# Kernel optimization log

Measured on AMD Instinct MI355X. Metric: run time of the kernel, lower is better.

Reference implementation:

```python
import jax, jax.numpy as jnp
import numpy as np

B, T = 128, 100
NOISE_STD = 0.1  # deterministic=False path

def leaky(x, slope):
    return jnp.where(x >= 0, x, slope * x)

def setup_inputs() -> dict:
    key = jax.random.key(0)
    ks = jax.random.split(key, 24)
    s = 0.02
    d = {}
    d["input_data"] = jax.random.normal(ks[0], (B, T, 3, 3), jnp.float32)
    d["eps"] = jax.random.normal(ks[1], (B, 64), jnp.float32)
    d["noise_eps"] = jax.random.normal(ks[2], (T, B, 4), jnp.float32)
    d["proj_W"] = jax.random.normal(ks[3], (4096, 9), jnp.float32) * s
    d["proj_b"] = jnp.zeros((4096,), jnp.float32)
    d["lstm_Wih"] = jax.random.normal(ks[4], (512, 4096), jnp.float32) * s
    d["lstm_Whh"] = jax.random.normal(ks[5], (512, 128), jnp.float32) * s
    d["lstm_bih"] = jnp.zeros((512,), jnp.float32)
    d["lstm_bhh"] = jnp.zeros((512,), jnp.float32)
    d["mu_W"] = jax.random.normal(ks[6], (64, 128), jnp.float32) * s
    d["mu_b"] = jnp.zeros((64,), jnp.float32)
    d["lv_W"] = jax.random.normal(ks[7], (64, 128), jnp.float32) * s
    d["lv_b"] = jnp.zeros((64,), jnp.float32)
    d["fcin_W"] = jax.random.normal(ks[8], (256, 64), jnp.float32) * s
    d["fcin_b"] = jnp.zeros((256,), jnp.float32)
    d["gru_Wih"] = jax.random.normal(ks[9], (783, 261), jnp.float32) * s
    d["gru_Whh"] = jax.random.normal(ks[10], (783, 261), jnp.float32) * s
    d["gru_bih"] = jnp.zeros((783,), jnp.float32)
    d["gru_bhh"] = jnp.zeros((783,), jnp.float32)
    d["jf_W1"] = jax.random.normal(ks[11], (64, 261), jnp.float32) * s
    d["jf_b1"] = jnp.zeros((64,), jnp.float32)
    d["jf_W2"] = jax.random.normal(ks[12], (9, 64), jnp.float32) * s
    d["jf_b2"] = jnp.zeros((9,), jnp.float32)
    return d

def reference(input_data, eps, noise_eps, proj_W, proj_b, lstm_Wih, lstm_Whh,
              lstm_bih, lstm_bhh, mu_W, mu_b, lv_W, lv_b, fcin_W, fcin_b,
              gru_Wih, gru_Whh, gru_bih, gru_bhh, jf_W1, jf_b1, jf_W2, jf_b2):
    b, t = input_data.shape[0], input_data.shape[1]
    pose = input_data.reshape(b, t, 9)
    # pose_projection: Linear(9, 4096) + LeakyReLU(0.1)
    proj = leaky(jnp.einsum('btj,kj->btk', pose, proj_W) + proj_b, 0.1)  # (B,T,4096)

    # LSTM over time, take final hidden state. PyTorch gate order: i,f,g,o.
    # Precompute input projections for all steps.
    x_gates = jnp.einsum('btk,gk->tbg', proj, lstm_Wih) + lstm_bih + lstm_bhh  # (T,B,512)
    hdim = 128
    def lstm_step(carry, xg):
        h, c = carry
        g = xg + h @ lstm_Whh.T  # (B,512)
        i, f, gg, o = jnp.split(g, 4, axis=-1)
        i, f, o = jax.nn.sigmoid(i), jax.nn.sigmoid(f), jax.nn.sigmoid(o)
        c = f * c + i * jnp.tanh(gg)
        h = o * jnp.tanh(c)
        return (h, c), None
    h0 = jnp.zeros((b, hdim), proj.dtype)
    (h_T, _), _ = jax.lax.scan(lstm_step, (h0, h0), x_gates)

    # VAE head (dropout in eval mode = identity)
    mu = leaky(h_T @ mu_W.T + mu_b, 0.1)
    logvar = jnp.clip(leaky(h_T @ lv_W.T + lv_b, 0.1), -10.0, 10.0)
    std = jnp.exp(0.5 * logvar)
    embedding = mu + eps * std

    x = embedding @ fcin_W.T + fcin_b  # (B,256)

    # Decoder GRU loop. PyTorch gate order: r,z,n; h' = (1-z)*n + z*h.
    noise = noise_eps * NOISE_STD  # (T,B,4)
    time_steps = (jnp.arange(t, dtype=x.dtype) / (t - 1))[:, None, None] * jnp.ones((t, b, 1), x.dtype)
    inp_seq = jnp.concatenate([jnp.broadcast_to(x[None], (t, b, 256)), noise, time_steps], axis=-1)  # (T,B,261)
    gx_seq = jnp.einsum('tbk,gk->tbg', inp_seq, gru_Wih) + gru_bih  # (T,B,783)

    def gru_step(h, gx):
        gh = h @ gru_Whh.T + gru_bhh
        gx_r, gx_z, gx_n = jnp.split(gx, 3, axis=-1)
        gh_r, gh_z, gh_n = jnp.split(gh, 3, axis=-1)
        r = jax.nn.sigmoid(gx_r + gh_r)
        z = jax.nn.sigmoid(gx_z + gh_z)
        n = jnp.tanh(gx_n + r * gh_n)
        h = (1.0 - z) * n + z * h
        frame = jax.nn.sigmoid(leaky(h @ jf_W1.T + jf_b1, 0.2) @ jf_W2.T + jf_b2)
        return h, frame

    h0g = jnp.zeros((b, 261), x.dtype)
    _, frames = jax.lax.scan(gru_step, h0g, gx_seq)  # (T,B,9)
    outputs = frames.transpose(1, 0, 2).reshape(b, t, 3, 3)
    return outputs, mu, logvar
```

## Files before the change

### kernel.cpp

```cpp
#include <hip/hip_runtime.h>
#include <hip/hip_bf16.h>

typedef float f32x4 __attribute__((ext_vector_type(4)));
typedef short s16x8 __attribute__((ext_vector_type(8)));

__device__ __forceinline__ float pv_sigm(float x){ return 1.0f/(1.0f + __expf(-x)); }
__device__ __forceinline__ float pv_tanh(float x){ float e = __expf(2.0f*x); return 1.0f - 2.0f/(e + 1.0f); }

__device__ __forceinline__ unsigned short pv_f2b(float x){
  union { float f; unsigned u; } c; c.f = x;
  unsigned r = (c.u + 0x7fffu + ((c.u >> 16) & 1u)) >> 16;
  return (unsigned short)r;
}
__device__ __forceinline__ unsigned pv_pack2(float a, float b){
  return ((unsigned)pv_f2b(b) << 16) | (unsigned)pv_f2b(a);
}
__device__ __forceinline__ float pv_lo(unsigned u){
  union { unsigned u; float f; } c; c.u = u << 16; return c.f;
}
__device__ __forceinline__ float pv_hi(unsigned u){
  union { unsigned u; float f; } c; c.u = u & 0xffff0000u; return c.f;
}

__device__ __forceinline__ unsigned char pv_fp8(float x){
  union { float f; unsigned u; } c; c.f = x;
  unsigned s = (c.u >> 24) & 0x80u;
  unsigned au = c.u & 0x7fffffffu;
  if (au == 0u) return (unsigned char)s;
  int ex = (int)(au >> 23) - 127;
  if (ex < -6) ex = -6;
  union { unsigned u; float f; } iv; iv.u = (unsigned)(3 - ex + 127) << 23;
  union { unsigned u; float f; } a;  a.u = au;
  int q = (int)rintf(a.f * iv.f);
  if (q >= 16) { q >>= 1; ex += 1; }
  unsigned bits;
  if (ex == -6 && q < 8) bits = (unsigned)q;
  else bits = (unsigned)(((ex + 7) << 3) | (q - 8));
  return (unsigned char)(s | bits);
}

#if defined(__has_builtin)
#if __has_builtin(__builtin_amdgcn_cvt_pk_fp8_f32)
#define PV_HW_FP8 1
#endif
#endif
__device__ __forceinline__ unsigned char pv_fp8_fast(float x){
#ifdef PV_HW_FP8
  return (unsigned char)__builtin_amdgcn_cvt_pk_fp8_f32(x, x, 0, false);
#else
  return pv_fp8(x);
#endif
}

__global__ void pv_prep_gru8(const float* Whh, const float* Wih,
                             unsigned long long* wfp8){
  int idx = blockIdx.x*256 + threadIdx.x;
  if (idx >= 29376) return;
  int T = idx / 576;
  int rem = idx - T*576;
  int c = rem >> 6;
  int l = rem & 63;
  int l16 = l & 15;
  int quad = l >> 4;
  int jb = T / 3;
  int ty = T - jb*3;
  int j = jb*16 + l16;
  int g = ty*261 + j;
  unsigned long long v = 0ull;
  #pragma unroll
  for (int e = 0; e < 8; ++e) {
    int k = c*32 + quad*8 + e;
    float w = 0.0f;
    if (j < 261) {
      if (k < 261) w = Whh[g*261 + k];
      else if (k < 266 && ty < 2) w = Wih[g*261 + 256 + (k - 261)];
    }
    v |= (unsigned long long)pv_fp8(8.0f*w) << (8*e);
  }
  wfp8[idx] = v;
}

__global__ __launch_bounds__(256) void pv_prep_wih(
    const float* __restrict__ Wih, unsigned* __restrict__ wihb)
{
  const int idx = blockIdx.x*256 + threadIdx.x;
  if (idx >= 262144) return;
  const float* src = Wih + idx*8;
  float4 a = *(const float4*)(src);
  float4 b = *(const float4*)(src + 4);
  uint4 o;
  o.x = pv_pack2(a.x, a.y);
  o.y = pv_pack2(a.z, a.w);
  o.z = pv_pack2(b.x, b.y);
  o.w = pv_pack2(b.z, b.w);
  *(uint4*)(wihb + idx*4) = o;
}

__global__ __launch_bounds__(512, 1) void pv_gemm4(
    const float* __restrict__ pose, const float* __restrict__ projW,
    const float* __restrict__ projb, const unsigned* __restrict__ wihb,
    const float* __restrict__ bih, const float* __restrict__ bhh,
    float* __restrict__ xg)
{
  __shared__ __align__(16) unsigned As2[128*20];
  __shared__ __align__(16) unsigned Bs2[2][256*20];
  __shared__ __align__(16) float Ws2[2][320];

  const int tid = threadIdx.x;
  const int m0 = blockIdx.x * 128;
  const int n0 = blockIdx.y * 256;
  const int wave = tid >> 6, lane = tid & 63;
  const int wm = wave >> 2, wn = wave & 3;
  const int l16 = lane & 15, quad = lane >> 4;
  const int rl = tid >> 2, kq = tid & 3;
  const int rb = tid >> 1, hb = tid & 1;

  float p[9];
  {
    const float* pr = pose + (m0 + rl)*9;
    #pragma unroll
    for (int j = 0; j < 9; ++j) p[j] = pr[j];
  }

  if (tid < 320) {
    Ws2[0][tid < 288 ? ((tid >> 5)*32 + (tid & 31)) : tid] =
        (tid < 288) ? projW[(tid & 31)*9 + (tid >> 5)] : projb[tid - 288];
  }
  {
    const unsigned* src = wihb + (n0 + rb)*2048 + hb*8;
    *(uint4*)(&Bs2[0][rb*20 + hb*8])     = *(const uint4*)(src);
    *(uint4*)(&Bs2[0][rb*20 + hb*8 + 4]) = *(const uint4*)(src + 4);
  }
  __syncthreads();

  f32x4 acc[4][4];
  #pragma unroll
  for (int i = 0; i < 4; ++i)
    #pragma unroll
    for (int j = 0; j < 4; ++j) acc[i][j] = (f32x4){0.f,0.f,0.f,0.f};

  for (int kk = 0; kk < 128; ++kk) {
    const int cur = kk & 1, nxt = cur ^ 1;
    const int kn = kk + 1;

    uint4 bn0, bn1; float wv = 0.0f;
    if (kn < 128) {
      const unsigned* bsrc = wihb + (n0 + rb)*2048 + kn*16 + hb*8;
      bn0 = *(const uint4*)(bsrc);
      bn1 = *(const uint4*)(bsrc + 4);
      if (tid < 320)
        wv = (tid < 288) ? projW[kn*288 + (tid & 31)*9 + (tid >> 5)]
                         : projb[kn*32 + (tid - 288)];
    }

    {
      const float* W = Ws2[cur];
      f32x4 slo = *(const f32x4*)(W + 288 + kq*8);
      f32x4 shi = *(const f32x4*)(W + 292 + kq*8);
      #pragma unroll
      for (int j = 0; j < 9; ++j) {
        f32x4 wlo = *(const f32x4*)(W + j*32 + kq*8);
        f32x4 whi = *(const f32x4*)(W + j*32 + kq*8 + 4);
        slo += p[j]*wlo;
        shi += p[j]*whi;
      }
      #pragma unroll
      for (int e = 0; e < 4; ++e) {
        slo[e] = fmaxf(slo[e], 0.1f*slo[e]);
        shi[e] = fmaxf(shi[e], 0.1f*shi[e]);
      }
      uint4 av;
      av.x = pv_pack2(slo[0], slo[1]);
      av.y = pv_pack2(slo[2], slo[3]);
      av.z = pv_pack2(shi[0], shi[1]);
      av.w = pv_pack2(shi[2], shi[3]);
      *(uint4*)(&As2[rl*20 + kq*4]) = av;
    }
    __syncthreads();

    {
      const unsigned short* As16 = (const unsigned short*)As2;
      const unsigned short* Bs16 = (const unsigned short*)Bs2[cur];
      s16x8 af[4];
      #pragma unroll
      for (int i = 0; i < 4; ++i)
        af[i] = *(const s16x8*)(As16 + (wm*64 + i*16 + l16)*40 + quad*8);
      #pragma unroll
      for (int j = 0; j < 4; ++j) {
        s16x8 bv = *(const s16x8*)(Bs16 + (wn*64 + j*16 + l16)*40 + quad*8);
        #pragma unroll
        for (int i = 0; i < 4; ++i)
          acc[i][j] = __builtin_amdgcn_mfma_f32_16x16x32_bf16(af[i], bv, acc[i][j], 0, 0, 0);
      }
    }

    if (kn < 128) {
      *(uint4*)(&Bs2[nxt][rb*20 + hb*8])     = bn0;
      *(uint4*)(&Bs2[nxt][rb*20 + hb*8 + 4]) = bn1;
      if (tid < 320)
        Ws2[nxt][tid < 288 ? ((tid >> 5)*32 + (tid & 31)) : tid] = wv;
    }
    __syncthreads();
  }

  #pragma unroll
  for (int j = 0; j < 4; ++j) {
    int col = n0 + wn*64 + j*16 + l16;
    float bsum = bih[col] + bhh[col];
    #pragma unroll
    for (int i = 0; i < 4; ++i) {
      #pragma unroll
      for (int r = 0; r < 4; ++r) {
        int row = m0 + wm*64 + i*16 + quad*4 + r;
        int bb = row / 100;
        int tt = row - bb*100;
        xg[(tt*128 + bb)*512 + col] = acc[i][j][r] + bsum;
      }
    }
  }
}

__global__ __launch_bounds__(256) void pv_gemm(
    const float* pose, const float* projW, const float* projb,
    const float* Wih, const float* bih, const float* bhh,
    float* xg)
{
  __shared__ __align__(16) unsigned As[128*24];
  __shared__ __align__(16) unsigned Bs[128*24];
  __shared__ float Ws[320];

  const int tid = threadIdx.x;
  const int m0 = blockIdx.x * 128;
  const int n0 = blockIdx.y * 128;

  const int rl = tid >> 1;
  const int kh = tid & 1;
  float p0,p1,p2,p3,p4,p5,p6,p7,p8;
  {
    const float* pr = pose + (m0 + rl) * 9;
    p0=pr[0]; p1=pr[1]; p2=pr[2]; p3=pr[3]; p4=pr[4];
    p5=pr[5]; p6=pr[6]; p7=pr[7]; p8=pr[8];
  }

  const int wave = tid >> 6;
  const int lane = tid & 63;
  const int wm = wave >> 1, wn = wave & 1;
  const int l16 = lane & 15, quad = lane >> 4;

  f32x4 acc[4][4];
  #pragma unroll
  for (int i = 0; i < 4; ++i)
    #pragma unroll
    for (int j = 0; j < 4; ++j) acc[i][j] = (f32x4){0.f,0.f,0.f,0.f};

  for (int kk = 0; kk < 128; ++kk) {
    __syncthreads();
    for (int idx = tid; idx < 320; idx += 256)
      Ws[idx] = (idx < 288) ? projW[kk*288 + idx] : projb[kk*32 + (idx - 288)];
    #pragma unroll
    for (int i = 0; i < 8; ++i) {
      int q = tid + i*256;
      int nl = q >> 4;
      int kp = q & 15;
      const float* src = Wih + (n0 + nl)*4096 + kk*32 + kp*2;
      Bs[nl*24 + kp] = pv_pack2(src[0], src[1]);
    }
    __syncthreads();
    {
      const int kbase = kh*16;
      const float* wbase = Ws + kbase*9;
      float av[16];
      #pragma unroll
      for (int u = 0; u < 16; ++u) {
        const float* wr = wbase + u*9;
        float s = Ws[288 + kbase + u]
                + p0*wr[0] + p1*wr[1] + p2*wr[2] + p3*wr[3] + p4*wr[4]
                + p5*wr[5] + p6*wr[6] + p7*wr[7] + p8*wr[8];
        av[u] = fmaxf(s, 0.1f*s);
      }
      #pragma unroll
      for (int q = 0; q < 8; ++q)
        As[rl*24 + kh*8 + q] = pv_pack2(av[2*q], av[2*q+1]);
    }
    __syncthreads();
    const unsigned short* As16 = (const unsigned short*)As;
    const unsigned short* Bs16 = (const unsigned short*)Bs;
    s16x8 af[4], bfv[4];
    #pragma unroll
    for (int i = 0; i < 4; ++i)
      af[i] = *(const s16x8*)(As16 + (wm*64 + i*16 + l16)*48 + quad*8);
    #pragma unroll
    for (int j = 0; j < 4; ++j)
      bfv[j] = *(const s16x8*)(Bs16 + (wn*64 + j*16 + l16)*48 + quad*8);
    #pragma unroll
    for (int i = 0; i < 4; ++i)
      #pragma unroll
      for (int j = 0; j < 4; ++j)
        acc[i][j] = __builtin_amdgcn_mfma_f32_16x16x32_bf16(af[i], bfv[j], acc[i][j], 0, 0, 0);
  }
  #pragma unroll
  for (int j = 0; j < 4; ++j) {
    int col = n0 + wn*64 + j*16 + l16;
    float bsum = bih[col] + bhh[col];
    #pragma unroll
    for (int i = 0; i < 4; ++i) {
      #pragma unroll
      for (int r = 0; r < 4; ++r) {
        int row = m0 + wm*64 + i*16 + quad*4 + r;
        int bb = row / 100;
        int tt = row - bb*100;
        xg[(tt*128 + bb)*512 + col] = acc[i][j][r] + bsum;
      }
    }
  }
}

__global__ __launch_bounds__(512, 1) void pv_lstm2(
    const float* __restrict__ xg, const float* __restrict__ Whh,
    float* __restrict__ hT)
{
  __shared__ __align__(16) unsigned short Hs2[2][16*136];
  const int tid = threadIdx.x;
  const int wv = tid >> 6;
  const int lane = tid & 63;
  const int l16 = lane & 15, quad = lane >> 4;
  const int m0 = blockIdx.x * 16;
  const int j = wv*16 + l16;

  s16x8 bfr[4][4];
  #pragma unroll
  for (int ty = 0; ty < 4; ++ty) {
    const int g = ty*128 + j;
    #pragma unroll
    for (int c = 0; c < 4; ++c) {
      s16x8 v;
      #pragma unroll
      for (int e = 0; e < 8; ++e)
        v[e] = (short)pv_f2b(Whh[g*128 + c*32 + quad*8 + e]);
      bfr[ty][c] = v;
    }
  }
  for (int i = tid; i < 2*16*136; i += 512) ((unsigned short*)Hs2)[i] = 0;

  float cst[4] = {0.f, 0.f, 0.f, 0.f};
  const float* xbase = xg + (m0 + quad*4)*512 + j;

  float xv[4][4];
  #pragma unroll
  for (int r = 0; r < 4; ++r)
    #pragma unroll
    for (int ty = 0; ty < 4; ++ty)
      xv[r][ty] = xbase[(0*128 + r)*512 + ty*128];
  __syncthreads();

  for (int t = 0; t < 100; ++t) {
    const int cur = t & 1, nxt = cur ^ 1;
    float xn[4][4];
    if (t < 99) {
      #pragma unroll
      for (int r = 0; r < 4; ++r)
        #pragma unroll
        for (int ty = 0; ty < 4; ++ty)
          xn[r][ty] = xbase[((t+1)*128 + r)*512 + ty*128];
    }
    f32x4 acc[4];
    #pragma unroll
    for (int ty = 0; ty < 4; ++ty) acc[ty] = (f32x4){0.f,0.f,0.f,0.f};
    #pragma unroll
    for (int c = 0; c < 4; ++c) {
      s16x8 a = *(const s16x8*)(&Hs2[cur][l16*136 + c*32 + quad*8]);
      #pragma unroll
      for (int ty = 0; ty < 4; ++ty)
        acc[ty] = __builtin_amdgcn_mfma_f32_16x16x32_bf16(a, bfr[ty][c], acc[ty], 0, 0, 0);
    }
    #pragma unroll
    for (int r = 0; r < 4; ++r) {
      float gi = acc[0][r] + xv[r][0];
      float gf = acc[1][r] + xv[r][1];
      float gg = acc[2][r] + xv[r][2];
      float go = acc[3][r] + xv[r][3];
      float c_ = pv_sigm(gf)*cst[r] + pv_sigm(gi)*pv_tanh(gg);
      cst[r] = c_;
      float h = pv_sigm(go)*pv_tanh(c_);
      Hs2[nxt][(quad*4 + r)*136 + j] = pv_f2b(h);
      if (t == 99) hT[(m0 + quad*4 + r)*128 + j] = h;
    }
    if (t < 99) {
      #pragma unroll
      for (int r = 0; r < 4; ++r)
        #pragma unroll
        for (int ty = 0; ty < 4; ++ty)
          xv[r][ty] = xn[r][ty];
    }
    __syncthreads();
  }
}

__global__ __launch_bounds__(64) void pv_head(
    const float* hT, const float* eps,
    const float* muW, const float* mub,
    const float* lvW, const float* lvb,
    const float* fcW, const float* fcb,
    float* xvec, float* out)
{
  __shared__ float hrow[128];
  __shared__ float emb[64];
  const int b = blockIdx.x, j = threadIdx.x;
  hrow[j] = hT[b*128 + j];
  hrow[j + 64] = hT[b*128 + 64 + j];
  __syncthreads();
  float sm = mub[j], sl = lvb[j];
  for (int k = 0; k < 128; ++k) {
    sm += hrow[k]*muW[j*128 + k];
    sl += hrow[k]*lvW[j*128 + k];
  }
  float mu = fmaxf(sm, 0.1f*sm);
  float lv = fmaxf(sl, 0.1f*sl);
  lv = fminf(fmaxf(lv, -10.0f), 10.0f);
  float em = mu + eps[b*64 + j]*__expf(0.5f*lv);
  emb[j] = em;
  out[115200 + b*64 + j] = mu;
  out[123392 + b*64 + j] = lv;
  __syncthreads();
  for (int c4 = 0; c4 < 4; ++c4) {
    int c = c4*64 + j;
    float s = fcb[c];
    for (int k = 0; k < 64; ++k) s += emb[k]*fcW[c*64 + k];
    xvec[b*256 + c] = s;
  }
}

__global__ __launch_bounds__(256) void pv_gxbase(
    const float* xvec, const float* Wih,
    const float* bih, const float* bhh, float* gxb)
{
  __shared__ float xs[8*256];
  const int tid = threadIdx.x;
  const int bg = blockIdx.x;
  const int gg = blockIdx.y;
  for (int i = tid; i < 2048; i += 256) xs[i] = xvec[bg*2048 + i];
  __syncthreads();
  const int g = gg*256 + tid;
  if (g >= 783) return;
  float bias = bih[g] + ((g < 522) ? bhh[g] : 0.0f);
  float a0=bias,a1=bias,a2=bias,a3=bias,a4=bias,a5=bias,a6=bias,a7=bias;
  const float* wr = Wih + g*261;
  for (int k = 0; k < 256; ++k) {
    float w = wr[k];
    a0 += xs[0*256 + k]*w; a1 += xs[1*256 + k]*w;
    a2 += xs[2*256 + k]*w; a3 += xs[3*256 + k]*w;
    a4 += xs[4*256 + k]*w; a5 += xs[5*256 + k]*w;
    a6 += xs[6*256 + k]*w; a7 += xs[7*256 + k]*w;
  }
  gxb[(bg*8 + 0)*783 + g] = a0; gxb[(bg*8 + 1)*783 + g] = a1;
  gxb[(bg*8 + 2)*783 + g] = a2; gxb[(bg*8 + 3)*783 + g] = a3;
  gxb[(bg*8 + 4)*783 + g] = a4; gxb[(bg*8 + 5)*783 + g] = a5;
  gxb[(bg*8 + 6)*783 + g] = a6; gxb[(bg*8 + 7)*783 + g] = a7;
}

__global__ __launch_bounds__(512, 1) void pv_gru5(
    const float* __restrict__ gxb, const unsigned long long* __restrict__ wfp8,
    const float* __restrict__ Wih, const float* __restrict__ bhh,
    const float* __restrict__ noise, float* __restrict__ hseq)
{
  __shared__ __align__(16) unsigned long long Bl[27*9*64];
  __shared__ __align__(16) unsigned char A2[16*296];
  __shared__ __align__(16) float Ds[4*792];
  const int tid = threadIdx.x;
  const int wv = tid >> 6;
  const int lane = tid & 63;
  const int l16 = lane & 15, quad = lane >> 4;
  const int m0 = blockIdx.x * 4;
  const int tailOwner = (wv >= 5);

  long bfr[3][9];
  #pragma unroll
  for (int s = 0; s < 3; ++s)
    #pragma unroll
    for (int c = 0; c < 9; ++c)
      bfr[s][c] = (long)wfp8[((3*wv + s)*9 + c)*64 + lane];
  #pragma unroll
  for (int s = 0; s < 3; ++s)
    #pragma unroll
    for (int c = 0; c < 9; ++c)
      asm volatile("" : "+v"(bfr[s][c]));

  const int r_u = tid & 3;
  const int j1 = tid >> 2;
  const int j2 = 128 + j1;
  const int hasE3 = (tid < 20);
  const int j3 = 256 + (tid >> 2);
  float gx1[3], gx2[3], gx3[3], wn1[5], wn2[5], wn3[5];
  float bh1, bh2, bh3 = 0.f, h1 = 0.f, h2 = 0.f, h3 = 0.f;
  {
    const float* gb = gxb + (m0 + r_u)*783;
    gx1[0] = gb[j1]; gx1[1] = gb[261 + j1]; gx1[2] = gb[522 + j1];
    gx2[0] = gb[j2]; gx2[1] = gb[261 + j2]; gx2[2] = gb[522 + j2];
    const float* w1 = Wih + (522 + j1)*261 + 256;
    wn1[0] = 0.1f*w1[0]; wn1[1] = 0.1f*w1[1]; wn1[2] = 0.1f*w1[2];
    wn1[3] = 0.1f*w1[3]; wn1[4] = w1[4];
    const float* w2 = Wih + (522 + j2)*261 + 256;
    wn2[0] = 0.1f*w2[0]; wn2[1] = 0.1f*w2[1]; wn2[2] = 0.1f*w2[2];
    wn2[3] = 0.1f*w2[3]; wn2[4] = w2[4];
    bh1 = bhh[522 + j1];
    bh2 = bhh[522 + j2];
    #pragma unroll
    for (int k = 0; k < 3; ++k) gx3[k] = 0.f;
    #pragma unroll
    for (int k = 0; k < 5; ++k) wn3[k] = 0.f;
    if (hasE3) {
      gx3[0] = gb[j3]; gx3[1] = gb[261 + j3]; gx3[2] = gb[522 + j3];
      const float* w3 = Wih + (522 + j3)*261 + 256;
      wn3[0] = 0.1f*w3[0]; wn3[1] = 0.1f*w3[1]; wn3[2] = 0.1f*w3[2];
      wn3[3] = 0.1f*w3[3]; wn3[4] = w3[4];
      bh3 = bhh[522 + j3];
    }
  }

  for (int i = tid; i < 27*9*64; i += 512) Bl[i] = wfp8[24*9*64 + i];
  for (int i = tid; i < 4736; i += 512) A2[i] = 0;
  __syncthreads();
  if (tid < 20) {
    const int m = tid/5, i = tid - (tid/5)*5;
    float v = (i < 4) ? noise[(m0 + m)*4 + i]*0.1f : 0.0f;
    A2[m*296 + 261 + i] = pv_fp8(4.0f*v);
  }
  __syncthreads();

  const float inv32 = 1.0f/32.0f;
  const float* nptr = noise + (m0 + r_u)*4;
  for (int t = 0; t < 100; ++t) {
    const float4 ne = *(const float4*)(nptr + t*512);

    f32x4 acc[7];
    #pragma unroll
    for (int s = 0; s < 7; ++s) acc[s] = (f32x4){0,0,0,0};
    #pragma unroll
    for (int c = 0; c < 9; ++c) {
      const long a = *(const long*)(&A2[l16*296 + c*32 + quad*8]);
      acc[0] = __builtin_amdgcn_mfma_f32_16x16x32_fp8_fp8(a, bfr[0][c], acc[0], 0, 0, 0);
      acc[1] = __builtin_amdgcn_mfma_f32_16x16x32_fp8_fp8(a, bfr[1][c], acc[1], 0, 0, 0);
      acc[2] = __builtin_amdgcn_mfma_f32_16x16x32_fp8_fp8(a, bfr[2][c], acc[2], 0, 0, 0);
      const long b3 = (long)Bl[((3*wv + 0)*9 + c)*64 + lane];
      const long b4 = (long)Bl[((3*wv + 1)*9 + c)*64 + lane];
      const long b5 = (long)Bl[((3*wv + 2)*9 + c)*64 + lane];
      acc[3] = __builtin_amdgcn_mfma_f32_16x16x32_fp8_fp8(a, b3, acc[3], 0, 0, 0);
      acc[4] = __builtin_amdgcn_mfma_f32_16x16x32_fp8_fp8(a, b4, acc[4], 0, 0, 0);
      acc[5] = __builtin_amdgcn_mfma_f32_16x16x32_fp8_fp8(a, b5, acc[5], 0, 0, 0);
      if (tailOwner) {
        const long b6 = (long)Bl[((24 + (wv - 5))*9 + c)*64 + lane];
        acc[6] = __builtin_amdgcn_mfma_f32_16x16x32_fp8_fp8(a, b6, acc[6], 0, 0, 0);
      }
    }
    if (quad == 0) {
      #pragma unroll
      for (int s = 0; s < 3; ++s) {
        const int g = s*261 + wv*16 + l16;
        #pragma unroll
        for (int r = 0; r < 4; ++r) Ds[r*792 + g] = acc[s][r];
      }
      #pragma unroll
      for (int s = 0; s < 3; ++s) {
        const int g = s*261 + (8 + wv)*16 + l16;
        #pragma unroll
        for (int r = 0; r < 4; ++r) Ds[r*792 + g] = acc[3 + s][r];
      }
      if (tailOwner && l16 < 5) {
        const int g = (wv - 5)*261 + 256 + l16;
        #pragma unroll
        for (int r = 0; r < 4; ++r) Ds[r*792 + g] = acc[6][r];
      }
    }
    __syncthreads();

    {
      const float tv = (float)t * (1.0f/99.0f);
      const float* dsr = Ds + r_u*792;
      {
        float Dr = dsr[j1]*inv32 + gx1[0];
        float Dz = dsr[261 + j1]*inv32 + gx1[1];
        float Dn = dsr[522 + j1]*inv32;
        float nterm = ne.x*wn1[0] + ne.y*wn1[1] + ne.z*wn1[2]
                    + ne.w*wn1[3] + tv*wn1[4];
        float r_ = pv_sigm(Dr);
        float z_ = pv_sigm(Dz);
        float n_ = pv_tanh(gx1[2] + nterm + r_*(Dn + bh1));
        h1 = (1.0f - z_)*n_ + z_*h1;
        hseq[(t*128 + m0 + r_u)*261 + j1] = h1;
        A2[r_u*296 + j1] = pv_fp8_fast(4.0f*h1);
      }
      {
        float Dr = dsr[j2]*inv32 + gx2[0];
        float Dz = dsr[261 + j2]*inv32 + gx2[1];
        float Dn = dsr[522 + j2]*inv32;
        float nterm = ne.x*wn2[0] + ne.y*wn2[1] + ne.z*wn2[2]
                    + ne.w*wn2[3] + tv*wn2[4];
        float r_ = pv_sigm(Dr);
        float z_ = pv_sigm(Dz);
        float n_ = pv_tanh(gx2[2] + nterm + r_*(Dn + bh2));
        h2 = (1.0f - z_)*n_ + z_*h2;
        hseq[(t*128 + m0 + r_u)*261 + j2] = h2;
        A2[r_u*296 + j2] = pv_fp8_fast(4.0f*h2);
      }
      if (hasE3) {
        float Dr = dsr[j3]*inv32 + gx3[0];
        float Dz = dsr[261 + j3]*inv32 + gx3[1];
        float Dn = dsr[522 + j3]*inv32;
        float nterm = ne.x*wn3[0] + ne.y*wn3[1] + ne.z*wn3[2]
                    + ne.w*wn3[3] + tv*wn3[4];
        float r_ = pv_sigm(Dr);
        float z_ = pv_sigm(Dz);
        float n_ = pv_tanh(gx3[2] + nterm + r_*(Dn + bh3));
        h3 = (1.0f - z_)*n_ + z_*h3;
        hseq[(t*128 + m0 + r_u)*261 + j3] = h3;
        A2[r_u*296 + j3] = pv_fp8_fast(4.0f*h3);
      }
    }
    if (t < 99 && tid >= 40 && tid < 60) {
      const int k = tid - 40;
      const int m = k/5, i = k - (k/5)*5;
      float v = (i < 4) ? noise[((t+1)*128 + m0 + m)*4 + i]*0.1f
                        : (t+1)*(1.0f/99.0f);
      A2[m*296 + 261 + i] = pv_fp8(4.0f*v);
    }
    __syncthreads();
  }
}

__global__ __launch_bounds__(256) void pv_frames(
    const float* hseq, const float* W1, const float* b1,
    const float* W2, const float* b2, float* out)
{
  __shared__ __align__(16) float h16[16*264];
  __shared__ unsigned w1p[64*133];
  __shared__ float f1s[16*66];
  __shared__ float w2s[576];
  const int tid = threadIdx.x;
  const int r0 = blockIdx.x * 16;
  for (int i = tid; i < 16*264; i += 256) {
    int r = i / 264, k = i - r*264;
    h16[i] = (k < 261) ? hseq[(r0 + r)*261 + k] : 0.0f;
  }
  for (int i = tid; i < 64*131; i += 256) {
    int c = i/131, kp = i - (i/131)*131;
    int k = kp*2;
    float a0 = W1[c*261 + k];
    float a1 = (k + 1 < 261) ? W1[c*261 + k + 1] : 0.0f;
    w1p[c*133 + kp] = pv_pack2(a0, a1);
  }
  for (int i = tid; i < 576; i += 256) w2s[i] = W2[i];
  __syncthreads();
  #pragma unroll
  for (int e = 0; e < 4; ++e) {
    const int el = tid + e*256;
    const int r = el >> 6, c = el & 63;
    float s = b1[c];
    const unsigned* wp = w1p + c*133;
    const float* hr = h16 + r*264;
    for (int kp = 0; kp < 131; ++kp) {
      unsigned w = wp[kp];
      s += pv_lo(w)*hr[2*kp] + pv_hi(w)*hr[2*kp + 1];
    }
    f1s[r*66 + c] = fmaxf(s, 0.2f*s);
  }
  __syncthreads();
  if (tid < 144) {
    const int r = tid/9, oc = tid - (tid/9)*9;
    float s = b2[oc];
    const float* fr = f1s + r*66;
    const float* w = w2s + oc*64;
    #pragma unroll 8
    for (int k = 0; k < 64; ++k) s += fr[k]*w[k];
    const int rt = r0 + r;
    const int tt = rt >> 7, bb = rt & 127;
    out[bb*900 + tt*9 + oc] = pv_sigm(s);
  }
}

extern "C" __attribute__((visibility("default")))
void kernel_launch(void* const* d_in, const int* in_sizes, int n_in,
                   void* d_out, int out_size, void* d_ws, size_t ws_size,
                   hipStream_t stream)
{
  (void)in_sizes; (void)n_in; (void)out_size;
  const float* input_data = (const float*)d_in[0];
  const float* eps        = (const float*)d_in[1];
  const float* noise_eps  = (const float*)d_in[2];
  const float* proj_W     = (const float*)d_in[3];
  const float* proj_b     = (const float*)d_in[4];
  const float* lstm_Wih   = (const float*)d_in[5];
  const float* lstm_Whh   = (const float*)d_in[6];
  const float* lstm_bih   = (const float*)d_in[7];
  const float* lstm_bhh   = (const float*)d_in[8];
  const float* mu_W       = (const float*)d_in[9];
  const float* mu_b       = (const float*)d_in[10];
  const float* lv_W       = (const float*)d_in[11];
  const float* lv_b       = (const float*)d_in[12];
  const float* fcin_W     = (const float*)d_in[13];
  const float* fcin_b     = (const float*)d_in[14];
  const float* gru_Wih    = (const float*)d_in[15];
  const float* gru_Whh    = (const float*)d_in[16];
  const float* gru_bih    = (const float*)d_in[17];
  const float* gru_bhh    = (const float*)d_in[18];
  const float* jf_W1      = (const float*)d_in[19];
  const float* jf_b1      = (const float*)d_in[20];
  const float* jf_W2      = (const float*)d_in[21];
  const float* jf_b2      = (const float*)d_in[22];

  char* w = (char*)d_ws;
  float*              xg   = (float*)(w);
  unsigned long long* wfp8 = (unsigned long long*)(w + 26214400);
  float*              hT   = (float*)(w + 26449408);
  float*              xvec = (float*)(w + 26514944);
  float*              gxb  = (float*)(w + 26646016);
  float*              hseq = (float*)(w + 27046912);
  unsigned*           wihb = (unsigned*)(w + 40410112);
  float*              outf = (float*)d_out;

  const int use_split = (ws_size >= (size_t)44604416ull);

  pv_prep_gru8<<<115, 256, 0, stream>>>(gru_Whh, gru_Wih, wfp8);
  if (use_split) {
    pv_prep_wih<<<1024, 256, 0, stream>>>(lstm_Wih, wihb);
    pv_gemm4<<<dim3(100, 2), 512, 0, stream>>>(input_data, proj_W, proj_b, wihb,
                                               lstm_bih, lstm_bhh, xg);
  } else {
    pv_gemm<<<dim3(100, 4), 256, 0, stream>>>(input_data, proj_W, proj_b,
                                              lstm_Wih, lstm_bih, lstm_bhh, xg);
  }
  pv_lstm2<<<8, 512, 0, stream>>>(xg, lstm_Whh, hT);
  pv_head<<<128, 64, 0, stream>>>(hT, eps, mu_W, mu_b, lv_W, lv_b,
                                  fcin_W, fcin_b, xvec, outf);
  pv_gxbase<<<dim3(16, 4), 256, 0, stream>>>(xvec, gru_Wih, gru_bih, gru_bhh, gxb);
  pv_gru5<<<32, 512, 0, stream>>>(gxb, wfp8, gru_Wih, gru_bhh, noise_eps, hseq);
  pv_frames<<<800, 256, 0, stream>>>(hseq, jf_W1, jf_b1, jf_W2, jf_b2, outf);
}
```

Before: 747.8 us.

## Split LSTM batch across 32 blocks with 4 rows each and LDS gate exchange

The LSTM recurrence kernel now gives each block 4 batch rows instead of 16, launching 32 blocks instead of 8 to use more CUs. The MFMA still computes a 16-row tile, but only rows from quad 0 are valid; those gate pre-activations go through shared memory so that every thread does the elementwise cell update for one (row, unit) pair. This adds an extra barrier per step and a single-buffered H, in exchange for 4x less serial elementwise work per thread and more parallelism across the chip.

```diff
diff --git a/kernel.cpp b/kernel.cpp
--- a/kernel.cpp
+++ b/kernel.cpp
@@ -315,16 +315,17 @@
   }
 }
 
-__global__ __launch_bounds__(512, 1) void pv_lstm2(
+__global__ __launch_bounds__(512, 1) void pv_lstm3(
     const float* __restrict__ xg, const float* __restrict__ Whh,
     float* __restrict__ hT)
 {
-  __shared__ __align__(16) unsigned short Hs2[2][16*136];
+  __shared__ __align__(16) unsigned short Hs[16*136];
+  __shared__ __align__(16) float Ds[4*512];
   const int tid = threadIdx.x;
   const int wv = tid >> 6;
   const int lane = tid & 63;
   const int l16 = lane & 15, quad = lane >> 4;
-  const int m0 = blockIdx.x * 16;
+  const int m0 = blockIdx.x * 4;
   const int j = wv*16 + l16;
 
   s16x8 bfr[4][4];
@@ -340,57 +341,59 @@
       bfr[ty][c] = v;
     }
   }
-  for (int i = tid; i < 2*16*136; i += 512) ((unsigned short*)Hs2)[i] = 0;
-
-  float cst[4] = {0.f, 0.f, 0.f, 0.f};
-  const float* xbase = xg + (m0 + quad*4)*512 + j;
-
-  float xv[4][4];
-  #pragma unroll
-  for (int r = 0; r < 4; ++r)
-    #pragma unroll
-    for (int ty = 0; ty < 4; ++ty)
-      xv[r][ty] = xbase[(0*128 + r)*512 + ty*128];
+  for (int i = tid; i < 16*136; i += 512) Hs[i] = 0;
+
+  const int r_u = tid >> 7;
+  const int j_u = tid & 127;
+  float cst = 0.0f;
+  const float* xbase = xg + (m0 + r_u)*512 + j_u;
+
+  float xv[4];
+  #pragma unroll
+  for (int ty = 0; ty < 4; ++ty) xv[ty] = xbase[ty*128];
   __syncthreads();
 
   for (int t = 0; t < 100; ++t) {
-    const int cur = t & 1, nxt = cur ^ 1;
-    float xn[4][4];
+    float xn[4];
     if (t < 99) {
       #pragma unroll
-      for (int r = 0; r < 4; ++r)
-        #pragma unroll
-        for (int ty = 0; ty < 4; ++ty)
-          xn[r][ty] = xbase[((t+1)*128 + r)*512 + ty*128];
+      for (int ty = 0; ty < 4; ++ty)
+        xn[ty] = xbase[(t+1)*65536 + ty*128];
     }
     f32x4 acc[4];
     #pragma unroll
     for (int ty = 0; ty < 4; ++ty) acc[ty] = (f32x4){0.f,0.f,0.f,0.f};
     #pragma unroll
     for (int c = 0; c < 4; ++c) {
-      s16x8 a = *(const s16x8*)(&Hs2[cur][l16*136 + c*32 + quad*8]);
+      s16x8 a = *(const s16x8*)(&Hs[l16*136 + c*32 + quad*8]);
       #pragma unroll
       for (int ty = 0; ty < 4; ++ty)
         acc[ty] = __builtin_amdgcn_mfma_f32_16x16x32_bf16(a, bfr[ty][c], acc[ty], 0, 0, 0);
     }
-    #pragma unroll
-    for (int r = 0; r < 4; ++r) {
-      float gi = acc[0][r] + xv[r][0];
-      float gf = acc[1][r] + xv[r][1];
-      float gg = acc[2][r] + xv[r][2];
-      float go = acc[3][r] + xv[r][3];
-      float c_ = pv_sigm(gf)*cst[r] + pv_sigm(gi)*pv_tanh(gg);
-      cst[r] = c_;
+    if (quad == 0) {
+      #pragma unroll
+      for (int ty = 0; ty < 4; ++ty)
+        #pragma unroll
+        for (int r = 0; r < 4; ++r)
+          Ds[r*512 + ty*128 + j] = acc[ty][r];
+    }
+    __syncthreads();
+
+    {
+      const float* dsr = Ds + r_u*512;
+      float gi = dsr[j_u]       + xv[0];
+      float gf = dsr[128 + j_u] + xv[1];
+      float gg = dsr[256 + j_u] + xv[2];
+      float go = dsr[384 + j_u] + xv[3];
+      float c_ = pv_sigm(gf)*cst + pv_sigm(gi)*pv_tanh(gg);
+      cst = c_;
       float h = pv_sigm(go)*pv_tanh(c_);
-      Hs2[nxt][(quad*4 + r)*136 + j] = pv_f2b(h);
-      if (t == 99) hT[(m0 + quad*4 + r)*128 + j] = h;
+      Hs[r_u*136 + j_u] = pv_f2b(h);
+      if (t == 99) hT[(m0 + r_u)*128 + j_u] = h;
     }
     if (t < 99) {
       #pragma unroll
-      for (int r = 0; r < 4; ++r)
-        #pragma unroll
-        for (int ty = 0; ty < 4; ++ty)
-          xv[r][ty] = xn[r][ty];
+      for (int ty = 0; ty < 4; ++ty) xv[ty] = xn[ty];
     }
     __syncthreads();
   }
@@ -728,7 +731,7 @@
     pv_gemm<<<dim3(100, 4), 256, 0, stream>>>(input_data, proj_W, proj_b,
                                               lstm_Wih, lstm_bih, lstm_bhh, xg);
   }
-  pv_lstm2<<<8, 512, 0, stream>>>(xg, lstm_Whh, hT);
+  pv_lstm3<<<32, 512, 0, stream>>>(xg, lstm_Whh, hT);
   pv_head<<<128, 64, 0, stream>>>(hT, eps, mu_W, mu_b, lv_W, lv_b,
                                   fcin_W, fcin_b, xvec, outf);
   pv_gxbase<<<dim3(16, 4), 256, 0, stream>>>(xvec, gru_Wih, gru_bih, gru_bhh, gxb);
```

Result: faster. 678.7 us (median of 2 runs) (-9.2%).
